# Kernel tuning notes

Measured on AMD Instinct MI355X. Metric: run time of the kernel, lower is better.

The kernel has to match this reference:

```python
import jax, jax.numpy as jnp
import numpy as np

N_NODES = 100000
N_EDGES = 1600000
IN_CH = 128
EMB = 64


def _init_linear(key, fan_in, fan_out):
    kw, kb = jax.random.split(key)
    scale = 1.0 / np.sqrt(fan_in)
    W = jax.random.uniform(kw, (fan_in, fan_out), jnp.float32, -scale, scale)
    b = jax.random.uniform(kb, (fan_out,), jnp.float32, -scale, scale)
    return W, b


def setup_inputs() -> dict:
    key = jax.random.key(0)
    ks = jax.random.split(key, 6)
    x = jax.random.normal(ks[0], (N_NODES, IN_CH), jnp.float32)
    edge_index = jax.random.randint(ks[1], (2, N_EDGES), 0, N_NODES)
    batch = jnp.zeros((N_NODES,), jnp.int32)
    # conv1 MLP: in_channels -> 32 -> 64 ; conv2 MLP: 64 -> 64 -> embedding_dim
    W1, b1 = _init_linear(ks[2], IN_CH, 32)
    W2, b2 = _init_linear(ks[3], 32, 64)
    W3, b3 = _init_linear(ks[4], 64, 64)
    W4, b4 = _init_linear(ks[5], 64, EMB)
    return {"x": x, "edge_index": edge_index, "batch": batch,
            "W1": W1, "b1": b1, "W2": W2, "b2": b2,
            "W3": W3, "b3": b3, "W4": W4, "b4": b4}


def _mlp(h, Wa, ba, Wb, bb):
    # PyG MLP: Linear -> act -> Linear (plain last layer)
    return jax.nn.relu(h @ Wa + ba) @ Wb + bb


def _gin_conv(x, src, dst, Wa, ba, Wb, bb):
    # out_i = MLP((1+eps)*x_i + sum_{j->i} x_j), eps = 0 (GINConv default)
    agg = jax.ops.segment_sum(x[src], dst, num_segments=N_NODES)  # [N, d]
    return _mlp(x + agg, Wa, ba, Wb, bb)


def reference(x, edge_index, batch, W1, b1, W2, b2, W3, b3, W4, b4):
    src, dst = edge_index[0], edge_index[1]
    h = jax.nn.relu(_gin_conv(x, src, dst, W1, b1, W2, b2))  # [N, 64]
    h = jax.nn.relu(_gin_conv(h, src, dst, W3, b3, W4, b4))  # [N, EMB]
    # batch is overwritten with zeros in the original forward -> single graph
    pooled = jnp.mean(h, axis=0, keepdims=True)  # [1, EMB]
    return h, pooled
```

## Files before the change

kernel.cpp:

```cpp
#include <hip/hip_runtime.h>

#define NN 100000
#define NE 1600000
#define NLB 256
#define CHUNK (NE / NLB)
#define NB 196
#define BN 512

__device__ __forceinline__ float bf2f(unsigned short u) {
    return __uint_as_float(((unsigned int)u) << 16);
}
__device__ __forceinline__ unsigned short f2bf(float f) {
    unsigned int u = __float_as_uint(f);
    return (unsigned short)((u + 0x7FFFu + ((u >> 16) & 1u)) >> 16);
}

__global__ __launch_bounds__(256) void k_front(const int* __restrict__ src,
                                               const int* __restrict__ dst,
                                               int* __restrict__ pairs,
                                               int* __restrict__ tstart,
                                               int* __restrict__ tcnt,
                                               int* __restrict__ btot,
                                               const float* __restrict__ x,
                                               const float* __restrict__ W1,
                                               unsigned short* __restrict__ z1) {
    __shared__ float Ws[128 * 32];
    __shared__ float xs[32][129];
    __shared__ int cnt[NB];
    __shared__ int sc[256];
    __shared__ int cur[NB];
    int tid = threadIdx.x;
    if (blockIdx.x < NLB) {
        int blk = blockIdx.x;
        int e0 = blk * CHUNK;
        for (int i = tid; i < NB; i += 256) cnt[i] = 0;
        __syncthreads();
        for (int i = tid; i < CHUNK; i += 256) atomicAdd(&cnt[dst[e0 + i] >> 9], 1);
        __syncthreads();
        sc[tid] = (tid < NB) ? cnt[tid] : 0;
        __syncthreads();
        for (int off = 1; off < 256; off <<= 1) {
            int v = (tid >= off) ? sc[tid - off] : 0;
            __syncthreads();
            sc[tid] += v;
            __syncthreads();
        }
        if (tid < NB) {
            int excl = sc[tid] - cnt[tid];
            cur[tid] = excl;
            tstart[blk * NB + tid] = excl;
            tcnt[blk * NB + tid]   = cnt[tid];
            atomicAdd(&btot[tid], cnt[tid]);
        }
        __syncthreads();
        for (int i = tid; i < CHUNK; i += 256) {
            int d = dst[e0 + i], s = src[e0 + i];
            int p = atomicAdd(&cur[d >> 9], 1);
            pairs[e0 + p] = ((d & (BN - 1)) << 17) | s;
        }
    } else {
        int bid = blockIdx.x - NLB;
        for (int i = tid; i < 1024; i += 256) {
            float4 w = ((const float4*)W1)[i];
            float* d = &Ws[i * 4];
            d[0] = w.x; d[1] = w.y; d[2] = w.z; d[3] = w.w;
        }
        int n_loc = tid >> 3;
        int j0    = (tid & 7) * 4;
        for (int base = bid * 32; base < NN; base += 1024 * 32) {
            __syncthreads();
            for (int t = tid; t < 1024; t += 256) {
                int n = t >> 5, c = t & 31;
                float4 v = ((const float4*)(x + (size_t)(base + n) * 128))[c];
                float* d = &xs[n][c * 4];
                d[0] = v.x; d[1] = v.y; d[2] = v.z; d[3] = v.w;
            }
            __syncthreads();
            float a0 = 0.f, a1 = 0.f, a2 = 0.f, a3 = 0.f;
            #pragma unroll 8
            for (int k = 0; k < 128; k++) {
                float xv = xs[n_loc][k];
                float4 w = *(const float4*)&Ws[k * 32 + j0];
                a0 = fmaf(xv, w.x, a0); a1 = fmaf(xv, w.y, a1);
                a2 = fmaf(xv, w.z, a2); a3 = fmaf(xv, w.w, a3);
            }
            ushort4 o = { f2bf(a0), f2bf(a1), f2bf(a2), f2bf(a3) };
            *(ushort4*)&z1[(size_t)(base + n_loc) * 32 + j0] = o;
        }
    }
}

__global__ __launch_bounds__(1024) void k_build(const int* __restrict__ pairs,
                                                const int* __restrict__ tstart,
                                                const int* __restrict__ tcnt,
                                                const int* __restrict__ btot,
                                                int* __restrict__ csr,
                                                int* __restrict__ row,
                                                int* __restrict__ rend) {
    __shared__ int segS[NLB], segL[NLB];
    __shared__ int ncnt[BN];
    __shared__ int nbase[BN + 1];
    __shared__ int sc[256];
    __shared__ int sc2[256];
    __shared__ int base_s;
    int tid = threadIdx.x, b = blockIdx.x;

    if (tid < 256) sc2[tid] = (tid < NB) ? btot[tid] : 0;
    __syncthreads();
    for (int off = 1; off < 256; off <<= 1) {
        int v = 0;
        if (tid < 256 && tid >= off) v = sc2[tid - off];
        __syncthreads();
        if (tid < 256) sc2[tid] += v;
        __syncthreads();
    }
    if (tid == 0) base_s = (b == 0) ? 0 : sc2[b - 1];
    if (tid < NLB) {
        segS[tid] = tid * CHUNK + tstart[tid * NB + b];
        segL[tid] = tcnt[tid * NB + b];
    }
    for (int i = tid; i < BN; i += 1024) ncnt[i] = 0;
    __syncthreads();

    int wave = tid >> 6, lane = tid & 63;
    for (int s = wave; s < NLB; s += 16) {
        int st = segS[s], len = segL[s];
        for (int i = lane; i < len; i += 64)
            atomicAdd(&ncnt[pairs[st + i] >> 17], 1);
    }
    __syncthreads();

    int c0 = 0, c1 = 0, tsum = 0;
    if (tid < 256) { c0 = ncnt[2 * tid]; c1 = ncnt[2 * tid + 1]; tsum = c0 + c1; sc[tid] = tsum; }
    __syncthreads();
    for (int off = 1; off < 256; off <<= 1) {
        int v = 0;
        if (tid < 256 && tid >= off) v = sc[tid - off];
        __syncthreads();
        if (tid < 256) sc[tid] += v;
        __syncthreads();
    }
    if (tid < 256) {
        int excl = sc[tid] - tsum;
        nbase[2 * tid]     = excl;
        nbase[2 * tid + 1] = excl + c0;
        if (tid == 255) nbase[BN] = sc[255];
    }
    __syncthreads();

    int base = base_s;
    if (tid < BN) {
        int n = b * BN + tid;
        if (n < NN) { row[n] = base + nbase[tid]; rend[n] = base + nbase[tid + 1]; }
        ncnt[tid] = 0;
    }
    __syncthreads();

    for (int s = wave; s < NLB; s += 16) {
        int st = segS[s], len = segL[s];
        for (int i = lane; i < len; i += 64) {
            int p = pairs[st + i];
            int ln = p >> 17;
            int pos = atomicAdd(&ncnt[ln], 1);
            csr[base + nbase[ln] + pos] = p & 0x1FFFF;
        }
    }
}

__global__ __launch_bounds__(256) void k_gather32(const int* __restrict__ row,
                                                  const int* __restrict__ rend,
                                                  const int* __restrict__ csr,
                                                  const unsigned short* __restrict__ z,
                                                  float* __restrict__ agg) {
    int n = blockIdx.x * 4 + (threadIdx.x >> 6);
    int lane = threadIdx.x & 63;
    int g = lane >> 3;
    int q = lane & 7;
    int j = row[n], e = rend[n];
    float a0 = 0.f, a1 = 0.f, a2 = 0.f, a3 = 0.f;
#define G32_BODY(J) { \
        int idx_ = csr[(J) + g]; \
        uint2 v_ = *(const uint2*)(z + (size_t)idx_ * 32 + q * 4); \
        a0 += __uint_as_float(v_.x << 16); \
        a1 += __uint_as_float(v_.x & 0xFFFF0000u); \
        a2 += __uint_as_float(v_.y << 16); \
        a3 += __uint_as_float(v_.y & 0xFFFF0000u); }
    for (; j + 16 <= e; j += 16) { G32_BODY(j) G32_BODY(j + 8) }
    if (j + 8 <= e) { G32_BODY(j) j += 8; }
    int rem = e - j;
    if (rem > 0) {
        int gg = (g < rem) ? g : (rem - 1);
        int idx_ = csr[j + gg];
        uint2 v_ = *(const uint2*)(z + (size_t)idx_ * 32 + q * 4);
        if (g < rem) {
            a0 += __uint_as_float(v_.x << 16);
            a1 += __uint_as_float(v_.x & 0xFFFF0000u);
            a2 += __uint_as_float(v_.y << 16);
            a3 += __uint_as_float(v_.y & 0xFFFF0000u);
        }
    }
#undef G32_BODY
    #pragma unroll
    for (int m = 8; m < 64; m <<= 1) {
        a0 += __shfl_xor(a0, m);
        a1 += __shfl_xor(a1, m);
        a2 += __shfl_xor(a2, m);
        a3 += __shfl_xor(a3, m);
    }
    if (g == 0) *(float4*)&agg[(size_t)n * 32 + q * 4] = make_float4(a0, a1, a2, a3);
}

__global__ __launch_bounds__(256) void k_gather64(const int* __restrict__ row,
                                                  const int* __restrict__ rend,
                                                  const int* __restrict__ csr,
                                                  const unsigned short* __restrict__ z,
                                                  float* __restrict__ agg) {
    int n = blockIdx.x * 4 + (threadIdx.x >> 6);
    int lane = threadIdx.x & 63;
    int g = lane >> 3;
    int q = lane & 7;
    int j = row[n], e = rend[n];
    float a0 = 0.f, a1 = 0.f, a2 = 0.f, a3 = 0.f;
    float a4 = 0.f, a5 = 0.f, a6 = 0.f, a7 = 0.f;
#define G64_BODY(J) { \
        int idx_ = csr[(J) + g]; \
        uint4 v_ = *(const uint4*)(z + (size_t)idx_ * 64 + q * 8); \
        a0 += __uint_as_float(v_.x << 16); a1 += __uint_as_float(v_.x & 0xFFFF0000u); \
        a2 += __uint_as_float(v_.y << 16); a3 += __uint_as_float(v_.y & 0xFFFF0000u); \
        a4 += __uint_as_float(v_.z << 16); a5 += __uint_as_float(v_.z & 0xFFFF0000u); \
        a6 += __uint_as_float(v_.w << 16); a7 += __uint_as_float(v_.w & 0xFFFF0000u); }
    for (; j + 16 <= e; j += 16) { G64_BODY(j) G64_BODY(j + 8) }
    if (j + 8 <= e) { G64_BODY(j) j += 8; }
    int rem = e - j;
    if (rem > 0) {
        int gg = (g < rem) ? g : (rem - 1);
        int idx_ = csr[j + gg];
        uint4 v_ = *(const uint4*)(z + (size_t)idx_ * 64 + q * 8);
        if (g < rem) {
            a0 += __uint_as_float(v_.x << 16); a1 += __uint_as_float(v_.x & 0xFFFF0000u);
            a2 += __uint_as_float(v_.y << 16); a3 += __uint_as_float(v_.y & 0xFFFF0000u);
            a4 += __uint_as_float(v_.z << 16); a5 += __uint_as_float(v_.z & 0xFFFF0000u);
            a6 += __uint_as_float(v_.w << 16); a7 += __uint_as_float(v_.w & 0xFFFF0000u);
        }
    }
#undef G64_BODY
    #pragma unroll
    for (int m = 8; m < 64; m <<= 1) {
        a0 += __shfl_xor(a0, m); a1 += __shfl_xor(a1, m);
        a2 += __shfl_xor(a2, m); a3 += __shfl_xor(a3, m);
        a4 += __shfl_xor(a4, m); a5 += __shfl_xor(a5, m);
        a6 += __shfl_xor(a6, m); a7 += __shfl_xor(a7, m);
    }
    if (g == 0) {
        *(float4*)&agg[(size_t)n * 64 + q * 8]     = make_float4(a0, a1, a2, a3);
        *(float4*)&agg[(size_t)n * 64 + q * 8 + 4] = make_float4(a4, a5, a6, a7);
    }
}

__global__ __launch_bounds__(256) void k_mid(const unsigned short* __restrict__ z1,
                                             const float* __restrict__ agg1,
                                             const float* __restrict__ b1,
                                             const float* __restrict__ W2,
                                             const float* __restrict__ b2,
                                             const float* __restrict__ W3,
                                             unsigned short* __restrict__ z2) {
    __shared__ float W2s[32 * 64];
    __shared__ float W3s[64 * 64];
    __shared__ float ts[32][33];
    __shared__ float hs[32 * 68];
    __shared__ float b1s[32], b2s[64];
    for (int i = threadIdx.x; i < 512; i += 256) {
        float4 w = ((const float4*)W2)[i];
        float* d = &W2s[i * 4];
        d[0] = w.x; d[1] = w.y; d[2] = w.z; d[3] = w.w;
    }
    for (int i = threadIdx.x; i < 1024; i += 256) {
        float4 w = ((const float4*)W3)[i];
        float* d = &W3s[i * 4];
        d[0] = w.x; d[1] = w.y; d[2] = w.z; d[3] = w.w;
    }
    if (threadIdx.x < 32) b1s[threadIdx.x] = b1[threadIdx.x];
    if (threadIdx.x >= 64 && threadIdx.x < 128) b2s[threadIdx.x - 64] = b2[threadIdx.x - 64];
    int n2 = threadIdx.x >> 4;
    int j0 = (threadIdx.x & 15) * 4;
    int na = 2 * n2, nb = 2 * n2 + 1;
    for (int base = blockIdx.x * 32; base < NN; base += gridDim.x * 32) {
        __syncthreads();
        #pragma unroll
        for (int r = 0; r < 4; r++) {
            int idx = threadIdx.x + 256 * r;
            int n = idx >> 5, f = idx & 31;
            ts[n][f] = fmaxf(bf2f(z1[(size_t)base * 32 + idx]) + agg1[(size_t)base * 32 + idx] + b1s[f], 0.f);
        }
        __syncthreads();
        {
            float a00=0,a01=0,a02=0,a03=0,a10=0,a11=0,a12=0,a13=0;
            #pragma unroll 8
            for (int k = 0; k < 32; k++) {
                float t0 = ts[na][k], t1 = ts[nb][k];
                float4 w = *(const float4*)&W2s[k * 64 + j0];
                a00=fmaf(t0,w.x,a00); a01=fmaf(t0,w.y,a01); a02=fmaf(t0,w.z,a02); a03=fmaf(t0,w.w,a03);
                a10=fmaf(t1,w.x,a10); a11=fmaf(t1,w.y,a11); a12=fmaf(t1,w.z,a12); a13=fmaf(t1,w.w,a13);
            }
            *(float4*)&hs[na * 68 + j0] = make_float4(fmaxf(a00+b2s[j0],0.f), fmaxf(a01+b2s[j0+1],0.f),
                                                      fmaxf(a02+b2s[j0+2],0.f), fmaxf(a03+b2s[j0+3],0.f));
            *(float4*)&hs[nb * 68 + j0] = make_float4(fmaxf(a10+b2s[j0],0.f), fmaxf(a11+b2s[j0+1],0.f),
                                                      fmaxf(a12+b2s[j0+2],0.f), fmaxf(a13+b2s[j0+3],0.f));
        }
        __syncthreads();
        {
            float a00=0,a01=0,a02=0,a03=0,a10=0,a11=0,a12=0,a13=0;
            #pragma unroll 8
            for (int k = 0; k < 64; k++) {
                float h0 = hs[na * 68 + k], h1 = hs[nb * 68 + k];
                float4 w = *(const float4*)&W3s[k * 64 + j0];
                a00=fmaf(h0,w.x,a00); a01=fmaf(h0,w.y,a01); a02=fmaf(h0,w.z,a02); a03=fmaf(h0,w.w,a03);
                a10=fmaf(h1,w.x,a10); a11=fmaf(h1,w.y,a11); a12=fmaf(h1,w.z,a12); a13=fmaf(h1,w.w,a13);
            }
            ushort4 oa = { f2bf(a00), f2bf(a01), f2bf(a02), f2bf(a03) };
            ushort4 ob = { f2bf(a10), f2bf(a11), f2bf(a12), f2bf(a13) };
            *(ushort4*)&z2[(size_t)(base + na) * 64 + j0] = oa;
            *(ushort4*)&z2[(size_t)(base + nb) * 64 + j0] = ob;
        }
    }
}

__global__ __launch_bounds__(256) void k_final(const unsigned short* __restrict__ z2,
                                               const float* __restrict__ agg2,
                                               const float* __restrict__ b3,
                                               const float* __restrict__ W4,
                                               const float* __restrict__ b4,
                                               float* __restrict__ out,
                                               float* __restrict__ gpool) {
    __shared__ float W4s[64 * 64];
    __shared__ float us[32 * 68];
    __shared__ float b3s[64], b4s[64], pool[64];
    for (int i = threadIdx.x; i < 1024; i += 256) {
        float4 w = ((const float4*)W4)[i];
        float* d = &W4s[i * 4];
        d[0] = w.x; d[1] = w.y; d[2] = w.z; d[3] = w.w;
    }
    if (threadIdx.x < 64) { b3s[threadIdx.x] = b3[threadIdx.x]; pool[threadIdx.x] = 0.f; }
    if (threadIdx.x >= 64 && threadIdx.x < 128) b4s[threadIdx.x - 64] = b4[threadIdx.x - 64];
    int n2 = threadIdx.x >> 4;
    int j0 = (threadIdx.x & 15) * 4;
    int na = 2 * n2, nb = 2 * n2 + 1;
    float p0 = 0.f, p1 = 0.f, p2 = 0.f, p3 = 0.f;
    for (int base = blockIdx.x * 32; base < NN; base += gridDim.x * 32) {
        __syncthreads();
        #pragma unroll
        for (int r = 0; r < 8; r++) {
            int idx = threadIdx.x + 256 * r;
            int n = idx >> 6, f = idx & 63;
            us[n * 68 + f] = fmaxf(bf2f(z2[(size_t)base * 64 + idx]) + agg2[(size_t)base * 64 + idx] + b3s[f], 0.f);
        }
        __syncthreads();
        float a00=0,a01=0,a02=0,a03=0,a10=0,a11=0,a12=0,a13=0;
        #pragma unroll 8
        for (int k = 0; k < 64; k++) {
            float u0 = us[na * 68 + k], u1 = us[nb * 68 + k];
            float4 w = *(const float4*)&W4s[k * 64 + j0];
            a00=fmaf(u0,w.x,a00); a01=fmaf(u0,w.y,a01); a02=fmaf(u0,w.z,a02); a03=fmaf(u0,w.w,a03);
            a10=fmaf(u1,w.x,a10); a11=fmaf(u1,w.y,a11); a12=fmaf(u1,w.z,a12); a13=fmaf(u1,w.w,a13);
        }
        float v00=fmaxf(a00+b4s[j0],0.f), v01=fmaxf(a01+b4s[j0+1],0.f);
        float v02=fmaxf(a02+b4s[j0+2],0.f), v03=fmaxf(a03+b4s[j0+3],0.f);
        float v10=fmaxf(a10+b4s[j0],0.f), v11=fmaxf(a11+b4s[j0+1],0.f);
        float v12=fmaxf(a12+b4s[j0+2],0.f), v13=fmaxf(a13+b4s[j0+3],0.f);
        *(float4*)&out[(size_t)(base + na) * 64 + j0] = make_float4(v00, v01, v02, v03);
        *(float4*)&out[(size_t)(base + nb) * 64 + j0] = make_float4(v10, v11, v12, v13);
        p0 += v00 + v10; p1 += v01 + v11; p2 += v02 + v12; p3 += v03 + v13;
    }
    __syncthreads();
    atomicAdd(&pool[j0 + 0], p0);
    atomicAdd(&pool[j0 + 1], p1);
    atomicAdd(&pool[j0 + 2], p2);
    atomicAdd(&pool[j0 + 3], p3);
    __syncthreads();
    if (threadIdx.x < 64) unsafeAtomicAdd(&gpool[threadIdx.x], pool[threadIdx.x]);
}

__global__ void k_pool(const float* __restrict__ gpool, float* __restrict__ out) {
    int t = threadIdx.x;
    if (t < 64) out[(size_t)NN * 64 + t] = gpool[t] * (1.0f / NN);
}

extern "C" void kernel_launch(void* const* d_in, const int* in_sizes, int n_in,
                              void* d_out, int out_size, void* d_ws, size_t ws_size,
                              hipStream_t stream) {
    const float* x  = (const float*)d_in[0];
    const int*   ei = (const int*)d_in[1];
    const float* W1 = (const float*)d_in[3];
    const float* b1 = (const float*)d_in[4];
    const float* W2 = (const float*)d_in[5];
    const float* b2 = (const float*)d_in[6];
    const float* W3 = (const float*)d_in[7];
    const float* b3 = (const float*)d_in[8];
    const float* W4 = (const float*)d_in[9];
    const float* b4 = (const float*)d_in[10];
    float* out = (float*)d_out;

    int*   ip     = (int*)d_ws;
    int*   tstart = ip;
    int*   tcnt   = ip + NLB * NB;
    int*   btot   = ip + 2 * NLB * NB;
    float* gpool  = (float*)(ip + 2 * NLB * NB + 196);
    int*   row    = ip + 2 * NLB * NB + 260;
    int*   rend   = row + NN;
    int*   csr    = rend + NN;
    int*   pairs  = csr + NE;
    unsigned short* z1b = (unsigned short*)(pairs + NE);
    float* agg1   = (float*)(pairs + NE + NN * 16);
    float* agg2   = (float*)pairs;
    unsigned short* z2b = (unsigned short*)(agg1 + (size_t)NN * 32);
    const int* src = ei;
    const int* dst = ei + NE;

    hipMemsetAsync(btot, 0, (196 + 64) * sizeof(int), stream);
    k_front<<<NLB + 1024, 256, 0, stream>>>(src, dst, pairs, tstart, tcnt, btot, x, W1, z1b);
    k_build<<<NB, 1024, 0, stream>>>(pairs, tstart, tcnt, btot, csr, row, rend);
    k_gather32<<<NN / 4, 256, 0, stream>>>(row, rend, csr, z1b, agg1);
    k_mid<<<1024, 256, 0, stream>>>(z1b, agg1, b1, W2, b2, W3, z2b);
    k_gather64<<<NN / 4, 256, 0, stream>>>(row, rend, csr, z2b, agg2);
    k_final<<<1024, 256, 0, stream>>>(z2b, agg2, b3, W4, b4, out, gpool);
    k_pool<<<1, 64, 0, stream>>>(gpool, out);
}
```

Before: 312.1 us.

## Split layer-2 features into two halves to shrink gather working set

Stores the layer-2 bf16 node features as two separate 32-column tables and runs the neighbour gather as two passes, one per half, within a single launch. Each pass randomly reads a table half the size, which is meant to improve cache hit rates for the irregular gathers. In exchange, CSR indices and row bounds are read twice, twice as many blocks are launched, and the producer and consumer kernels use split addressing.

```diff
diff --git a/kernel.cpp b/kernel.cpp
--- a/kernel.cpp
+++ b/kernel.cpp
@@ -210,51 +210,51 @@
     if (g == 0) *(float4*)&agg[(size_t)n * 32 + q * 4] = make_float4(a0, a1, a2, a3);
 }
 
-__global__ __launch_bounds__(256) void k_gather64(const int* __restrict__ row,
-                                                  const int* __restrict__ rend,
-                                                  const int* __restrict__ csr,
-                                                  const unsigned short* __restrict__ z,
-                                                  float* __restrict__ agg) {
-    int n = blockIdx.x * 4 + (threadIdx.x >> 6);
+__global__ __launch_bounds__(256) void k_gather64h(const int* __restrict__ row,
+                                                   const int* __restrict__ rend,
+                                                   const int* __restrict__ csr,
+                                                   const unsigned short* __restrict__ z2a,
+                                                   const unsigned short* __restrict__ z2b,
+                                                   float* __restrict__ agg) {
+    int half = (blockIdx.x >= (NN / 4)) ? 1 : 0;
+    int blk  = blockIdx.x - half * (NN / 4);
+    const unsigned short* z = half ? z2b : z2a;
+    int n = blk * 4 + (threadIdx.x >> 6);
     int lane = threadIdx.x & 63;
     int g = lane >> 3;
     int q = lane & 7;
     int j = row[n], e = rend[n];
     float a0 = 0.f, a1 = 0.f, a2 = 0.f, a3 = 0.f;
-    float a4 = 0.f, a5 = 0.f, a6 = 0.f, a7 = 0.f;
-#define G64_BODY(J) { \
+#define GH_BODY(J) { \
         int idx_ = csr[(J) + g]; \
-        uint4 v_ = *(const uint4*)(z + (size_t)idx_ * 64 + q * 8); \
-        a0 += __uint_as_float(v_.x << 16); a1 += __uint_as_float(v_.x & 0xFFFF0000u); \
-        a2 += __uint_as_float(v_.y << 16); a3 += __uint_as_float(v_.y & 0xFFFF0000u); \
-        a4 += __uint_as_float(v_.z << 16); a5 += __uint_as_float(v_.z & 0xFFFF0000u); \
-        a6 += __uint_as_float(v_.w << 16); a7 += __uint_as_float(v_.w & 0xFFFF0000u); }
-    for (; j + 16 <= e; j += 16) { G64_BODY(j) G64_BODY(j + 8) }
-    if (j + 8 <= e) { G64_BODY(j) j += 8; }
+        uint2 v_ = *(const uint2*)(z + (size_t)idx_ * 32 + q * 4); \
+        a0 += __uint_as_float(v_.x << 16); \
+        a1 += __uint_as_float(v_.x & 0xFFFF0000u); \
+        a2 += __uint_as_float(v_.y << 16); \
+        a3 += __uint_as_float(v_.y & 0xFFFF0000u); }
+    for (; j + 16 <= e; j += 16) { GH_BODY(j) GH_BODY(j + 8) }
+    if (j + 8 <= e) { GH_BODY(j) j += 8; }
     int rem = e - j;
     if (rem > 0) {
         int gg = (g < rem) ? g : (rem - 1);
         int idx_ = csr[j + gg];
-        uint4 v_ = *(const uint4*)(z + (size_t)idx_ * 64 + q * 8);
+        uint2 v_ = *(const uint2*)(z + (size_t)idx_ * 32 + q * 4);
         if (g < rem) {
-            a0 += __uint_as_float(v_.x << 16); a1 += __uint_as_float(v_.x & 0xFFFF0000u);
-            a2 += __uint_as_float(v_.y << 16); a3 += __uint_as_float(v_.y & 0xFFFF0000u);
-            a4 += __uint_as_float(v_.z << 16); a5 += __uint_as_float(v_.z & 0xFFFF0000u);
-            a6 += __uint_as_float(v_.w << 16); a7 += __uint_as_float(v_.w & 0xFFFF0000u);
-        }
-    }
-#undef G64_BODY
+            a0 += __uint_as_float(v_.x << 16);
+            a1 += __uint_as_float(v_.x & 0xFFFF0000u);
+            a2 += __uint_as_float(v_.y << 16);
+            a3 += __uint_as_float(v_.y & 0xFFFF0000u);
+        }
+    }
+#undef GH_BODY
     #pragma unroll
     for (int m = 8; m < 64; m <<= 1) {
-        a0 += __shfl_xor(a0, m); a1 += __shfl_xor(a1, m);
-        a2 += __shfl_xor(a2, m); a3 += __shfl_xor(a3, m);
-        a4 += __shfl_xor(a4, m); a5 += __shfl_xor(a5, m);
-        a6 += __shfl_xor(a6, m); a7 += __shfl_xor(a7, m);
-    }
-    if (g == 0) {
-        *(float4*)&agg[(size_t)n * 64 + q * 8]     = make_float4(a0, a1, a2, a3);
-        *(float4*)&agg[(size_t)n * 64 + q * 8 + 4] = make_float4(a4, a5, a6, a7);
-    }
+        a0 += __shfl_xor(a0, m);
+        a1 += __shfl_xor(a1, m);
+        a2 += __shfl_xor(a2, m);
+        a3 += __shfl_xor(a3, m);
+    }
+    if (g == 0) *(float4*)&agg[(size_t)n * 64 + half * 32 + q * 4] = make_float4(a0, a1, a2, a3);
 }
 
 __global__ __launch_bounds__(256) void k_mid(const unsigned short* __restrict__ z1,
@@ -263,7 +263,8 @@
                                              const float* __restrict__ W2,
                                              const float* __restrict__ b2,
                                              const float* __restrict__ W3,
-                                             unsigned short* __restrict__ z2) {
+                                             unsigned short* __restrict__ z2a,
+                                             unsigned short* __restrict__ z2b) {
     __shared__ float W2s[32 * 64];
     __shared__ float W3s[64 * 64];
     __shared__ float ts[32][33];
@@ -284,6 +285,8 @@
     int n2 = threadIdx.x >> 4;
     int j0 = (threadIdx.x & 15) * 4;
     int na = 2 * n2, nb = 2 * n2 + 1;
+    unsigned short* zout = (j0 < 32) ? z2a : z2b;
+    int jj = j0 & 31;
     for (int base = blockIdx.x * 32; base < NN; base += gridDim.x * 32) {
         __syncthreads();
         #pragma unroll
@@ -319,13 +322,14 @@
             }
             ushort4 oa = { f2bf(a00), f2bf(a01), f2bf(a02), f2bf(a03) };
             ushort4 ob = { f2bf(a10), f2bf(a11), f2bf(a12), f2bf(a13) };
-            *(ushort4*)&z2[(size_t)(base + na) * 64 + j0] = oa;
-            *(ushort4*)&z2[(size_t)(base + nb) * 64 + j0] = ob;
-        }
-    }
-}
-
-__global__ __launch_bounds__(256) void k_final(const unsigned short* __restrict__ z2,
+            *(ushort4*)&zout[(size_t)(base + na) * 32 + jj] = oa;
+            *(ushort4*)&zout[(size_t)(base + nb) * 32 + jj] = ob;
+        }
+    }
+}
+
+__global__ __launch_bounds__(256) void k_final(const unsigned short* __restrict__ z2a,
+                                               const unsigned short* __restrict__ z2b,
                                                const float* __restrict__ agg2,
                                                const float* __restrict__ b3,
                                                const float* __restrict__ W4,
@@ -352,7 +356,9 @@
         for (int r = 0; r < 8; r++) {
             int idx = threadIdx.x + 256 * r;
             int n = idx >> 6, f = idx & 63;
-            us[n * 68 + f] = fmaxf(bf2f(z2[(size_t)base * 64 + idx]) + agg2[(size_t)base * 64 + idx] + b3s[f], 0.f);
+            const unsigned short* zsrc = (f < 32) ? z2a : z2b;
+            us[n * 68 + f] = fmaxf(bf2f(zsrc[(size_t)(base + n) * 32 + (f & 31)])
+                                   + agg2[(size_t)base * 64 + idx] + b3s[f], 0.f);
         }
         __syncthreads();
         float a00=0,a01=0,a02=0,a03=0,a10=0,a11=0,a12=0,a13=0;
@@ -412,7 +418,8 @@
     unsigned short* z1b = (unsigned short*)(pairs + NE);
     float* agg1   = (float*)(pairs + NE + NN * 16);
     float* agg2   = (float*)pairs;
-    unsigned short* z2b = (unsigned short*)(agg1 + (size_t)NN * 32);
+    unsigned short* z2a = (unsigned short*)(agg1 + (size_t)NN * 32);
+    unsigned short* z2bb = z2a + (size_t)NN * 32;
     const int* src = ei;
     const int* dst = ei + NE;
 
@@ -420,8 +427,8 @@
     k_front<<<NLB + 1024, 256, 0, stream>>>(src, dst, pairs, tstart, tcnt, btot, x, W1, z1b);
     k_build<<<NB, 1024, 0, stream>>>(pairs, tstart, tcnt, btot, csr, row, rend);
     k_gather32<<<NN / 4, 256, 0, stream>>>(row, rend, csr, z1b, agg1);
-    k_mid<<<1024, 256, 0, stream>>>(z1b, agg1, b1, W2, b2, W3, z2b);
-    k_gather64<<<NN / 4, 256, 0, stream>>>(row, rend, csr, z2b, agg2);
-    k_final<<<1024, 256, 0, stream>>>(z2b, agg2, b3, W4, b4, out, gpool);
+    k_mid<<<1024, 256, 0, stream>>>(z1b, agg1, b1, W2, b2, W3, z2a, z2bb);
+    k_gather64h<<<NN / 2, 256, 0, stream>>>(row, rend, csr, z2a, z2bb, agg2);
+    k_final<<<1024, 256, 0, stream>>>(z2a, z2bb, agg2, b3, W4, b4, out, gpool);
     k_pool<<<1, 64, 0, stream>>>(gpool, out);
 }
```

Result: slower. 332.1 us (+6.4%).

## Fuse neighbor gather-aggregation into MLP kernels via shared-memory staging

Applied to the files above, without the earlier changes.

The separate gather kernels for both GIN layers are removed. Each MLP block now gathers its 32 nodes' neighbor sums into shared memory before running the dense layers. This drops the fp32 agg buffers' global write and read round trip and two launches. The trade-off is that the gather phase now runs inside persistent 1024-block kernels with large shared-memory footprints, so occupancy and latency hiding for the irregular gathers may be lower, and gather and matmul phases serialize within a block.

```diff
diff --git a/kernel.cpp b/kernel.cpp
--- a/kernel.cpp
+++ b/kernel.cpp
@@ -167,130 +167,88 @@
     }
 }
 
-__global__ __launch_bounds__(256) void k_gather32(const int* __restrict__ row,
-                                                  const int* __restrict__ rend,
-                                                  const int* __restrict__ csr,
-                                                  const unsigned short* __restrict__ z,
-                                                  float* __restrict__ agg) {
-    int n = blockIdx.x * 4 + (threadIdx.x >> 6);
-    int lane = threadIdx.x & 63;
-    int g = lane >> 3;
-    int q = lane & 7;
-    int j = row[n], e = rend[n];
-    float a0 = 0.f, a1 = 0.f, a2 = 0.f, a3 = 0.f;
-#define G32_BODY(J) { \
-        int idx_ = csr[(J) + g]; \
-        uint2 v_ = *(const uint2*)(z + (size_t)idx_ * 32 + q * 4); \
-        a0 += __uint_as_float(v_.x << 16); \
-        a1 += __uint_as_float(v_.x & 0xFFFF0000u); \
-        a2 += __uint_as_float(v_.y << 16); \
-        a3 += __uint_as_float(v_.y & 0xFFFF0000u); }
-    for (; j + 16 <= e; j += 16) { G32_BODY(j) G32_BODY(j + 8) }
-    if (j + 8 <= e) { G32_BODY(j) j += 8; }
-    int rem = e - j;
-    if (rem > 0) {
-        int gg = (g < rem) ? g : (rem - 1);
-        int idx_ = csr[j + gg];
-        uint2 v_ = *(const uint2*)(z + (size_t)idx_ * 32 + q * 4);
-        if (g < rem) {
-            a0 += __uint_as_float(v_.x << 16);
-            a1 += __uint_as_float(v_.x & 0xFFFF0000u);
-            a2 += __uint_as_float(v_.y << 16);
-            a3 += __uint_as_float(v_.y & 0xFFFF0000u);
-        }
-    }
-#undef G32_BODY
-    #pragma unroll
-    for (int m = 8; m < 64; m <<= 1) {
-        a0 += __shfl_xor(a0, m);
-        a1 += __shfl_xor(a1, m);
-        a2 += __shfl_xor(a2, m);
-        a3 += __shfl_xor(a3, m);
-    }
-    if (g == 0) *(float4*)&agg[(size_t)n * 32 + q * 4] = make_float4(a0, a1, a2, a3);
-}
-
-__global__ __launch_bounds__(256) void k_gather64(const int* __restrict__ row,
-                                                  const int* __restrict__ rend,
-                                                  const int* __restrict__ csr,
-                                                  const unsigned short* __restrict__ z,
-                                                  float* __restrict__ agg) {
-    int n = blockIdx.x * 4 + (threadIdx.x >> 6);
-    int lane = threadIdx.x & 63;
-    int g = lane >> 3;
-    int q = lane & 7;
-    int j = row[n], e = rend[n];
-    float a0 = 0.f, a1 = 0.f, a2 = 0.f, a3 = 0.f;
-    float a4 = 0.f, a5 = 0.f, a6 = 0.f, a7 = 0.f;
-#define G64_BODY(J) { \
-        int idx_ = csr[(J) + g]; \
-        uint4 v_ = *(const uint4*)(z + (size_t)idx_ * 64 + q * 8); \
-        a0 += __uint_as_float(v_.x << 16); a1 += __uint_as_float(v_.x & 0xFFFF0000u); \
-        a2 += __uint_as_float(v_.y << 16); a3 += __uint_as_float(v_.y & 0xFFFF0000u); \
-        a4 += __uint_as_float(v_.z << 16); a5 += __uint_as_float(v_.z & 0xFFFF0000u); \
-        a6 += __uint_as_float(v_.w << 16); a7 += __uint_as_float(v_.w & 0xFFFF0000u); }
-    for (; j + 16 <= e; j += 16) { G64_BODY(j) G64_BODY(j + 8) }
-    if (j + 8 <= e) { G64_BODY(j) j += 8; }
-    int rem = e - j;
-    if (rem > 0) {
-        int gg = (g < rem) ? g : (rem - 1);
-        int idx_ = csr[j + gg];
-        uint4 v_ = *(const uint4*)(z + (size_t)idx_ * 64 + q * 8);
-        if (g < rem) {
-            a0 += __uint_as_float(v_.x << 16); a1 += __uint_as_float(v_.x & 0xFFFF0000u);
-            a2 += __uint_as_float(v_.y << 16); a3 += __uint_as_float(v_.y & 0xFFFF0000u);
-            a4 += __uint_as_float(v_.z << 16); a5 += __uint_as_float(v_.z & 0xFFFF0000u);
-            a6 += __uint_as_float(v_.w << 16); a7 += __uint_as_float(v_.w & 0xFFFF0000u);
-        }
-    }
-#undef G64_BODY
-    #pragma unroll
-    for (int m = 8; m < 64; m <<= 1) {
-        a0 += __shfl_xor(a0, m); a1 += __shfl_xor(a1, m);
-        a2 += __shfl_xor(a2, m); a3 += __shfl_xor(a3, m);
-        a4 += __shfl_xor(a4, m); a5 += __shfl_xor(a5, m);
-        a6 += __shfl_xor(a6, m); a7 += __shfl_xor(a7, m);
-    }
-    if (g == 0) {
-        *(float4*)&agg[(size_t)n * 64 + q * 8]     = make_float4(a0, a1, a2, a3);
-        *(float4*)&agg[(size_t)n * 64 + q * 8 + 4] = make_float4(a4, a5, a6, a7);
-    }
-}
-
-__global__ __launch_bounds__(256) void k_mid(const unsigned short* __restrict__ z1,
-                                             const float* __restrict__ agg1,
-                                             const float* __restrict__ b1,
-                                             const float* __restrict__ W2,
-                                             const float* __restrict__ b2,
-                                             const float* __restrict__ W3,
-                                             unsigned short* __restrict__ z2) {
+__global__ __launch_bounds__(256) void k_mid_g(const int* __restrict__ row,
+                                               const int* __restrict__ rend,
+                                               const int* __restrict__ csr,
+                                               const unsigned short* __restrict__ z1,
+                                               const float* __restrict__ b1,
+                                               const float* __restrict__ W2,
+                                               const float* __restrict__ b2,
+                                               const float* __restrict__ W3,
+                                               unsigned short* __restrict__ z2) {
     __shared__ float W2s[32 * 64];
     __shared__ float W3s[64 * 64];
     __shared__ float ts[32][33];
     __shared__ float hs[32 * 68];
+    __shared__ float aggs[32 * 32];
     __shared__ float b1s[32], b2s[64];
-    for (int i = threadIdx.x; i < 512; i += 256) {
+    int tid = threadIdx.x;
+    for (int i = tid; i < 512; i += 256) {
         float4 w = ((const float4*)W2)[i];
         float* d = &W2s[i * 4];
         d[0] = w.x; d[1] = w.y; d[2] = w.z; d[3] = w.w;
     }
-    for (int i = threadIdx.x; i < 1024; i += 256) {
+    for (int i = tid; i < 1024; i += 256) {
         float4 w = ((const float4*)W3)[i];
         float* d = &W3s[i * 4];
         d[0] = w.x; d[1] = w.y; d[2] = w.z; d[3] = w.w;
     }
-    if (threadIdx.x < 32) b1s[threadIdx.x] = b1[threadIdx.x];
-    if (threadIdx.x >= 64 && threadIdx.x < 128) b2s[threadIdx.x - 64] = b2[threadIdx.x - 64];
-    int n2 = threadIdx.x >> 4;
-    int j0 = (threadIdx.x & 15) * 4;
+    if (tid < 32) b1s[tid] = b1[tid];
+    if (tid >= 64 && tid < 128) b2s[tid - 64] = b2[tid - 64];
+    int wave = tid >> 6, lane = tid & 63;
+    int g = lane >> 3;
+    int q = lane & 7;
+    int n2 = tid >> 4;
+    int j0 = (tid & 15) * 4;
     int na = 2 * n2, nb = 2 * n2 + 1;
     for (int base = blockIdx.x * 32; base < NN; base += gridDim.x * 32) {
         __syncthreads();
-        #pragma unroll
-        for (int r = 0; r < 4; r++) {
-            int idx = threadIdx.x + 256 * r;
+        for (int rnd = 0; rnd < 8; rnd++) {
+            int nl = rnd * 4 + wave;
+            int n = base + nl;
+            int j = row[n], e = rend[n];
+            float a0 = 0.f, a1 = 0.f, a2 = 0.f, a3 = 0.f;
+#define G32B(J) { \
+            int idx_ = csr[(J) + g]; \
+            uint2 v_ = *(const uint2*)(z1 + (size_t)idx_ * 32 + q * 4); \
+            a0 += __uint_as_float(v_.x << 16); \
+            a1 += __uint_as_float(v_.x & 0xFFFF0000u); \
+            a2 += __uint_as_float(v_.y << 16); \
+            a3 += __uint_as_float(v_.y & 0xFFFF0000u); }
+            for (; j + 16 <= e; j += 16) { G32B(j) G32B(j + 8) }
+            if (j + 8 <= e) { G32B(j) j += 8; }
+            int rem = e - j;
+            if (rem > 0) {
+                int gg = (g < rem) ? g : (rem - 1);
+                int idx_ = csr[j + gg];
+                uint2 v_ = *(const uint2*)(z1 + (size_t)idx_ * 32 + q * 4);
+                if (g < rem) {
+                    a0 += __uint_as_float(v_.x << 16);
+                    a1 += __uint_as_float(v_.x & 0xFFFF0000u);
+                    a2 += __uint_as_float(v_.y << 16);
+                    a3 += __uint_as_float(v_.y & 0xFFFF0000u);
+                }
+            }
+#undef G32B
+            #pragma unroll
+            for (int m = 8; m < 64; m <<= 1) {
+                a0 += __shfl_xor(a0, m);
+                a1 += __shfl_xor(a1, m);
+                a2 += __shfl_xor(a2, m);
+                a3 += __shfl_xor(a3, m);
+            }
+            if (g == 0) *(float4*)&aggs[nl * 32 + q * 4] = make_float4(a0, a1, a2, a3);
+        }
+        __syncthreads();
+        {
+            int idx = tid * 4;
             int n = idx >> 5, f = idx & 31;
-            ts[n][f] = fmaxf(bf2f(z1[(size_t)base * 32 + idx]) + agg1[(size_t)base * 32 + idx] + b1s[f], 0.f);
+            ushort4 zv = *(const ushort4*)&z1[(size_t)base * 32 + idx];
+            float4 av = *(const float4*)&aggs[idx];
+            ts[n][f + 0] = fmaxf(bf2f(zv.x) + av.x + b1s[f + 0], 0.f);
+            ts[n][f + 1] = fmaxf(bf2f(zv.y) + av.y + b1s[f + 1], 0.f);
+            ts[n][f + 2] = fmaxf(bf2f(zv.z) + av.z + b1s[f + 2], 0.f);
+            ts[n][f + 3] = fmaxf(bf2f(zv.w) + av.w + b1s[f + 3], 0.f);
         }
         __syncthreads();
         {
@@ -325,34 +283,92 @@
     }
 }
 
-__global__ __launch_bounds__(256) void k_final(const unsigned short* __restrict__ z2,
-                                               const float* __restrict__ agg2,
-                                               const float* __restrict__ b3,
-                                               const float* __restrict__ W4,
-                                               const float* __restrict__ b4,
-                                               float* __restrict__ out,
-                                               float* __restrict__ gpool) {
+__global__ __launch_bounds__(256) void k_final_g(const int* __restrict__ row,
+                                                 const int* __restrict__ rend,
+                                                 const int* __restrict__ csr,
+                                                 const unsigned short* __restrict__ z2,
+                                                 const float* __restrict__ b3,
+                                                 const float* __restrict__ W4,
+                                                 const float* __restrict__ b4,
+                                                 float* __restrict__ out,
+                                                 float* __restrict__ gpool) {
     __shared__ float W4s[64 * 64];
     __shared__ float us[32 * 68];
+    __shared__ float aggs[32 * 64];
     __shared__ float b3s[64], b4s[64], pool[64];
-    for (int i = threadIdx.x; i < 1024; i += 256) {
+    int tid = threadIdx.x;
+    for (int i = tid; i < 1024; i += 256) {
         float4 w = ((const float4*)W4)[i];
         float* d = &W4s[i * 4];
         d[0] = w.x; d[1] = w.y; d[2] = w.z; d[3] = w.w;
     }
-    if (threadIdx.x < 64) { b3s[threadIdx.x] = b3[threadIdx.x]; pool[threadIdx.x] = 0.f; }
-    if (threadIdx.x >= 64 && threadIdx.x < 128) b4s[threadIdx.x - 64] = b4[threadIdx.x - 64];
-    int n2 = threadIdx.x >> 4;
-    int j0 = (threadIdx.x & 15) * 4;
+    if (tid < 64) { b3s[tid] = b3[tid]; pool[tid] = 0.f; }
+    if (tid >= 64 && tid < 128) b4s[tid - 64] = b4[tid - 64];
+    int wave = tid >> 6, lane = tid & 63;
+    int g = lane >> 3;
+    int q = lane & 7;
+    int n2 = tid >> 4;
+    int j0 = (tid & 15) * 4;
     int na = 2 * n2, nb = 2 * n2 + 1;
     float p0 = 0.f, p1 = 0.f, p2 = 0.f, p3 = 0.f;
     for (int base = blockIdx.x * 32; base < NN; base += gridDim.x * 32) {
         __syncthreads();
-        #pragma unroll
-        for (int r = 0; r < 8; r++) {
-            int idx = threadIdx.x + 256 * r;
+        for (int rnd = 0; rnd < 8; rnd++) {
+            int nl = rnd * 4 + wave;
+            int n = base + nl;
+            int j = row[n], e = rend[n];
+            float a0=0.f,a1=0.f,a2=0.f,a3=0.f,a4=0.f,a5=0.f,a6=0.f,a7=0.f;
+#define G64B(J) { \
+            int idx_ = csr[(J) + g]; \
+            uint4 v_ = *(const uint4*)(z2 + (size_t)idx_ * 64 + q * 8); \
+            a0 += __uint_as_float(v_.x << 16); a1 += __uint_as_float(v_.x & 0xFFFF0000u); \
+            a2 += __uint_as_float(v_.y << 16); a3 += __uint_as_float(v_.y & 0xFFFF0000u); \
+            a4 += __uint_as_float(v_.z << 16); a5 += __uint_as_float(v_.z & 0xFFFF0000u); \
+            a6 += __uint_as_float(v_.w << 16); a7 += __uint_as_float(v_.w & 0xFFFF0000u); }
+            for (; j + 16 <= e; j += 16) { G64B(j) G64B(j + 8) }
+            if (j + 8 <= e) { G64B(j) j += 8; }
+            int rem = e - j;
+            if (rem > 0) {
+                int gg = (g < rem) ? g : (rem - 1);
+                int idx_ = csr[j + gg];
+                uint4 v_ = *(const uint4*)(z2 + (size_t)idx_ * 64 + q * 8);
+                if (g < rem) {
+                    a0 += __uint_as_float(v_.x << 16); a1 += __uint_as_float(v_.x & 0xFFFF0000u);
+                    a2 += __uint_as_float(v_.y << 16); a3 += __uint_as_float(v_.y & 0xFFFF0000u);
+                    a4 += __uint_as_float(v_.z << 16); a5 += __uint_as_float(v_.z & 0xFFFF0000u);
+                    a6 += __uint_as_float(v_.w << 16); a7 += __uint_as_float(v_.w & 0xFFFF0000u);
+                }
+            }
+#undef G64B
+            #pragma unroll
+            for (int m = 8; m < 64; m <<= 1) {
+                a0 += __shfl_xor(a0, m); a1 += __shfl_xor(a1, m);
+                a2 += __shfl_xor(a2, m); a3 += __shfl_xor(a3, m);
+                a4 += __shfl_xor(a4, m); a5 += __shfl_xor(a5, m);
+                a6 += __shfl_xor(a6, m); a7 += __shfl_xor(a7, m);
+            }
+            if (g == 0) {
+                *(float4*)&aggs[nl * 64 + q * 8]     = make_float4(a0, a1, a2, a3);
+                *(float4*)&aggs[nl * 64 + q * 8 + 4] = make_float4(a4, a5, a6, a7);
+            }
+        }
+        __syncthreads();
+        {
+            int idx = tid * 8;
             int n = idx >> 6, f = idx & 63;
-            us[n * 68 + f] = fmaxf(bf2f(z2[(size_t)base * 64 + idx]) + agg2[(size_t)base * 64 + idx] + b3s[f], 0.f);
+            ushort4 zv0 = *(const ushort4*)&z2[(size_t)base * 64 + idx];
+            ushort4 zv1 = *(const ushort4*)&z2[(size_t)base * 64 + idx + 4];
+            float4 av0 = *(const float4*)&aggs[idx];
+            float4 av1 = *(const float4*)&aggs[idx + 4];
+            float* u = &us[n * 68 + f];
+            u[0] = fmaxf(bf2f(zv0.x) + av0.x + b3s[f + 0], 0.f);
+            u[1] = fmaxf(bf2f(zv0.y) + av0.y + b3s[f + 1], 0.f);
+            u[2] = fmaxf(bf2f(zv0.z) + av0.z + b3s[f + 2], 0.f);
+            u[3] = fmaxf(bf2f(zv0.w) + av0.w + b3s[f + 3], 0.f);
+            u[4] = fmaxf(bf2f(zv1.x) + av1.x + b3s[f + 4], 0.f);
+            u[5] = fmaxf(bf2f(zv1.y) + av1.y + b3s[f + 5], 0.f);
+            u[6] = fmaxf(bf2f(zv1.z) + av1.z + b3s[f + 6], 0.f);
+            u[7] = fmaxf(bf2f(zv1.w) + av1.w + b3s[f + 7], 0.f);
         }
         __syncthreads();
         float a00=0,a01=0,a02=0,a03=0,a10=0,a11=0,a12=0,a13=0;
@@ -377,7 +393,7 @@
     atomicAdd(&pool[j0 + 2], p2);
     atomicAdd(&pool[j0 + 3], p3);
     __syncthreads();
-    if (threadIdx.x < 64) unsafeAtomicAdd(&gpool[threadIdx.x], pool[threadIdx.x]);
+    if (tid < 64) unsafeAtomicAdd(&gpool[tid], pool[tid]);
 }
 
 __global__ void k_pool(const float* __restrict__ gpool, float* __restrict__ out) {
@@ -410,18 +426,14 @@
     int*   csr    = rend + NN;
     int*   pairs  = csr + NE;
     unsigned short* z1b = (unsigned short*)(pairs + NE);
-    float* agg1   = (float*)(pairs + NE + NN * 16);
-    float* agg2   = (float*)pairs;
-    unsigned short* z2b = (unsigned short*)(agg1 + (size_t)NN * 32);
+    unsigned short* z2b = z1b + (size_t)NN * 32;
     const int* src = ei;
     const int* dst = ei + NE;
 
     hipMemsetAsync(btot, 0, (196 + 64) * sizeof(int), stream);
     k_front<<<NLB + 1024, 256, 0, stream>>>(src, dst, pairs, tstart, tcnt, btot, x, W1, z1b);
     k_build<<<NB, 1024, 0, stream>>>(pairs, tstart, tcnt, btot, csr, row, rend);
-    k_gather32<<<NN / 4, 256, 0, stream>>>(row, rend, csr, z1b, agg1);
-    k_mid<<<1024, 256, 0, stream>>>(z1b, agg1, b1, W2, b2, W3, z2b);
-    k_gather64<<<NN / 4, 256, 0, stream>>>(row, rend, csr, z2b, agg2);
-    k_final<<<1024, 256, 0, stream>>>(z2b, agg2, b3, W4, b4, out, gpool);
+    k_mid_g<<<1024, 256, 0, stream>>>(row, rend, csr, z1b, b1, W2, b2, W3, z2b);
+    k_final_g<<<1024, 256, 0, stream>>>(row, rend, csr, z2b, b3, W4, b4, out, gpool);
     k_pool<<<1, 64, 0, stream>>>(gpool, out);
 }
```

After: 358.3 us. 14.8% more time.

## Split CSR neighbor lists by source half and gather layer-2 in two passes

Applied to the files above, without the earlier changes.

The CSR build now sorts each node's neighbors into two groups, sources below 50000 and sources at or above it, and records the split point per node. The second-layer gather runs as two launches: one over the low-source half and one over the high-source half, with the second pass adding into the first pass's result. Each pass then reads only half of the bf16 z2 table, so that working set is more likely to stay in cache. The cost is an extra launch, a second read and write of agg2, and slightly more bookkeeping in k_build. The rend array is also replaced by row[n+1], with a sentinel row[NN].

```diff
diff --git a/kernel.cpp b/kernel.cpp
--- a/kernel.cpp
+++ b/kernel.cpp
@@ -6,6 +6,7 @@
 #define CHUNK (NE / NLB)
 #define NB 196
 #define BN 512
+#define SRCMID 50000
 
 __device__ __forceinline__ float bf2f(unsigned short u) {
     return __uint_as_float(((unsigned int)u) << 16);
@@ -96,9 +97,10 @@
                                                 const int* __restrict__ btot,
                                                 int* __restrict__ csr,
                                                 int* __restrict__ row,
-                                                int* __restrict__ rend) {
+                                                int* __restrict__ mid) {
     __shared__ int segS[NLB], segL[NLB];
-    __shared__ int ncnt[BN];
+    __shared__ int cA[BN], cB[BN];
+    __shared__ int pA[BN], pB[BN];
     __shared__ int nbase[BN + 1];
     __shared__ int sc[256];
     __shared__ int sc2[256];
@@ -119,19 +121,26 @@
         segS[tid] = tid * CHUNK + tstart[tid * NB + b];
         segL[tid] = tcnt[tid * NB + b];
     }
-    for (int i = tid; i < BN; i += 1024) ncnt[i] = 0;
+    for (int i = tid; i < BN; i += 1024) { cA[i] = 0; cB[i] = 0; }
     __syncthreads();
 
     int wave = tid >> 6, lane = tid & 63;
     for (int s = wave; s < NLB; s += 16) {
         int st = segS[s], len = segL[s];
-        for (int i = lane; i < len; i += 64)
-            atomicAdd(&ncnt[pairs[st + i] >> 17], 1);
-    }
-    __syncthreads();
-
-    int c0 = 0, c1 = 0, tsum = 0;
-    if (tid < 256) { c0 = ncnt[2 * tid]; c1 = ncnt[2 * tid + 1]; tsum = c0 + c1; sc[tid] = tsum; }
+        for (int i = lane; i < len; i += 64) {
+            int p = pairs[st + i];
+            atomicAdd(((p & 0x1FFFF) < SRCMID) ? &cA[p >> 17] : &cB[p >> 17], 1);
+        }
+    }
+    __syncthreads();
+
+    int t0 = 0, tsum = 0;
+    if (tid < 256) {
+        t0 = cA[2 * tid] + cB[2 * tid];
+        int t1 = cA[2 * tid + 1] + cB[2 * tid + 1];
+        tsum = t0 + t1;
+        sc[tid] = tsum;
+    }
     __syncthreads();
     for (int off = 1; off < 256; off <<= 1) {
         int v = 0;
@@ -143,17 +152,21 @@
     if (tid < 256) {
         int excl = sc[tid] - tsum;
         nbase[2 * tid]     = excl;
-        nbase[2 * tid + 1] = excl + c0;
-        if (tid == 255) nbase[BN] = sc[255];
+        nbase[2 * tid + 1] = excl + t0;
     }
     __syncthreads();
 
     int base = base_s;
     if (tid < BN) {
         int n = b * BN + tid;
-        if (n < NN) { row[n] = base + nbase[tid]; rend[n] = base + nbase[tid + 1]; }
-        ncnt[tid] = 0;
-    }
+        if (n < NN) {
+            row[n] = base + nbase[tid];
+            mid[n] = base + nbase[tid] + cA[tid];
+        }
+        pA[tid] = 0;
+        pB[tid] = cA[tid];
+    }
+    if (b == NB - 1 && tid == 0) row[NN] = NE;
     __syncthreads();
 
     for (int s = wave; s < NLB; s += 16) {
@@ -161,14 +174,14 @@
         for (int i = lane; i < len; i += 64) {
             int p = pairs[st + i];
             int ln = p >> 17;
-            int pos = atomicAdd(&ncnt[ln], 1);
-            csr[base + nbase[ln] + pos] = p & 0x1FFFF;
+            int s_ = p & 0x1FFFF;
+            int pos = atomicAdd((s_ < SRCMID) ? &pA[ln] : &pB[ln], 1);
+            csr[base + nbase[ln] + pos] = s_;
         }
     }
 }
 
 __global__ __launch_bounds__(256) void k_gather32(const int* __restrict__ row,
-                                                  const int* __restrict__ rend,
                                                   const int* __restrict__ csr,
                                                   const unsigned short* __restrict__ z,
                                                   float* __restrict__ agg) {
@@ -176,7 +189,7 @@
     int lane = threadIdx.x & 63;
     int g = lane >> 3;
     int q = lane & 7;
-    int j = row[n], e = rend[n];
+    int j = row[n], e = row[n + 1];
     float a0 = 0.f, a1 = 0.f, a2 = 0.f, a3 = 0.f;
 #define G32_BODY(J) { \
         int idx_ = csr[(J) + g]; \
@@ -210,32 +223,34 @@
     if (g == 0) *(float4*)&agg[(size_t)n * 32 + q * 4] = make_float4(a0, a1, a2, a3);
 }
 
-__global__ __launch_bounds__(256) void k_gather64(const int* __restrict__ row,
-                                                  const int* __restrict__ rend,
-                                                  const int* __restrict__ csr,
-                                                  const unsigned short* __restrict__ z,
-                                                  float* __restrict__ agg) {
+__global__ __launch_bounds__(256) void k_gather64p(const int* __restrict__ row,
+                                                   const int* __restrict__ mid,
+                                                   const int* __restrict__ csr,
+                                                   const unsigned short* __restrict__ z2,
+                                                   float* __restrict__ agg,
+                                                   int phase) {
     int n = blockIdx.x * 4 + (threadIdx.x >> 6);
     int lane = threadIdx.x & 63;
     int g = lane >> 3;
     int q = lane & 7;
-    int j = row[n], e = rend[n];
+    int j = phase ? mid[n] : row[n];
+    int e = phase ? row[n + 1] : mid[n];
     float a0 = 0.f, a1 = 0.f, a2 = 0.f, a3 = 0.f;
     float a4 = 0.f, a5 = 0.f, a6 = 0.f, a7 = 0.f;
-#define G64_BODY(J) { \
+#define G64B(J) { \
         int idx_ = csr[(J) + g]; \
-        uint4 v_ = *(const uint4*)(z + (size_t)idx_ * 64 + q * 8); \
+        uint4 v_ = *(const uint4*)(z2 + (size_t)idx_ * 64 + q * 8); \
         a0 += __uint_as_float(v_.x << 16); a1 += __uint_as_float(v_.x & 0xFFFF0000u); \
         a2 += __uint_as_float(v_.y << 16); a3 += __uint_as_float(v_.y & 0xFFFF0000u); \
         a4 += __uint_as_float(v_.z << 16); a5 += __uint_as_float(v_.z & 0xFFFF0000u); \
         a6 += __uint_as_float(v_.w << 16); a7 += __uint_as_float(v_.w & 0xFFFF0000u); }
-    for (; j + 16 <= e; j += 16) { G64_BODY(j) G64_BODY(j + 8) }
-    if (j + 8 <= e) { G64_BODY(j) j += 8; }
+    for (; j + 16 <= e; j += 16) { G64B(j) G64B(j + 8) }
+    if (j + 8 <= e) { G64B(j) j += 8; }
     int rem = e - j;
     if (rem > 0) {
         int gg = (g < rem) ? g : (rem - 1);
         int idx_ = csr[j + gg];
-        uint4 v_ = *(const uint4*)(z + (size_t)idx_ * 64 + q * 8);
+        uint4 v_ = *(const uint4*)(z2 + (size_t)idx_ * 64 + q * 8);
         if (g < rem) {
             a0 += __uint_as_float(v_.x << 16); a1 += __uint_as_float(v_.x & 0xFFFF0000u);
             a2 += __uint_as_float(v_.y << 16); a3 += __uint_as_float(v_.y & 0xFFFF0000u);
@@ -243,7 +258,7 @@
             a6 += __uint_as_float(v_.w << 16); a7 += __uint_as_float(v_.w & 0xFFFF0000u);
         }
     }
-#undef G64_BODY
+#undef G64B
     #pragma unroll
     for (int m = 8; m < 64; m <<= 1) {
         a0 += __shfl_xor(a0, m); a1 += __shfl_xor(a1, m);
@@ -252,8 +267,17 @@
         a6 += __shfl_xor(a6, m); a7 += __shfl_xor(a7, m);
     }
     if (g == 0) {
-        *(float4*)&agg[(size_t)n * 64 + q * 8]     = make_float4(a0, a1, a2, a3);
-        *(float4*)&agg[(size_t)n * 64 + q * 8 + 4] = make_float4(a4, a5, a6, a7);
+        float4 r0 = make_float4(a0, a1, a2, a3);
+        float4 r1 = make_float4(a4, a5, a6, a7);
+        float* d0 = &agg[(size_t)n * 64 + q * 8];
+        if (phase) {
+            float4 o0 = *(const float4*)d0;
+            float4 o1 = *(const float4*)(d0 + 4);
+            r0.x += o0.x; r0.y += o0.y; r0.z += o0.z; r0.w += o0.w;
+            r1.x += o1.x; r1.y += o1.y; r1.z += o1.z; r1.w += o1.w;
+        }
+        *(float4*)d0 = r0;
+        *(float4*)(d0 + 4) = r1;
     }
 }
 
@@ -406,8 +430,8 @@
     int*   btot   = ip + 2 * NLB * NB;
     float* gpool  = (float*)(ip + 2 * NLB * NB + 196);
     int*   row    = ip + 2 * NLB * NB + 260;
-    int*   rend   = row + NN;
-    int*   csr    = rend + NN;
+    int*   mid    = row + NN + 4;
+    int*   csr    = mid + NN + 4;
     int*   pairs  = csr + NE;
     unsigned short* z1b = (unsigned short*)(pairs + NE);
     float* agg1   = (float*)(pairs + NE + NN * 16);
@@ -418,10 +442,11 @@
 
     hipMemsetAsync(btot, 0, (196 + 64) * sizeof(int), stream);
     k_front<<<NLB + 1024, 256, 0, stream>>>(src, dst, pairs, tstart, tcnt, btot, x, W1, z1b);
-    k_build<<<NB, 1024, 0, stream>>>(pairs, tstart, tcnt, btot, csr, row, rend);
-    k_gather32<<<NN / 4, 256, 0, stream>>>(row, rend, csr, z1b, agg1);
+    k_build<<<NB, 1024, 0, stream>>>(pairs, tstart, tcnt, btot, csr, row, mid);
+    k_gather32<<<NN / 4, 256, 0, stream>>>(row, csr, z1b, agg1);
     k_mid<<<1024, 256, 0, stream>>>(z1b, agg1, b1, W2, b2, W3, z2b);
-    k_gather64<<<NN / 4, 256, 0, stream>>>(row, rend, csr, z2b, agg2);
+    k_gather64p<<<NN / 4, 256, 0, stream>>>(row, mid, csr, z2b, agg2, 0);
+    k_gather64p<<<NN / 4, 256, 0, stream>>>(row, mid, csr, z2b, agg2, 1);
     k_final<<<1024, 256, 0, stream>>>(z2b, agg2, b3, W4, b4, out, gpool);
     k_pool<<<1, 64, 0, stream>>>(gpool, out);
 }
```

Result: slower. 337.5 us (+8.1%).
